# Kernel optimization log

Hardware: AMD Instinct MI355X
Metric: run time of the kernel (lower is better)

Reference implementation:

```python
import jax, jax.numpy as jnp
import numpy as np
from jax import lax

B, S, D, H = 4, 1024, 1024, 16
DK = D // H


def setup_inputs() -> dict:
    key = jax.random.key(0)
    ks = jax.random.split(key, 8)
    s = 0.02
    return {
        "text_embeddings": jax.random.normal(ks[0], (B, S, D), jnp.float32),
        "text_mask": jnp.ones((B, S), jnp.int32),
        "W_G": jax.random.normal(ks[1], (D, D), jnp.float32) * s,
        "b_G": jnp.zeros((D,), jnp.float32),
        "Wq": jax.random.normal(ks[2], (D, D), jnp.float32) * s,
        "bq": jnp.zeros((D,), jnp.float32),
        "Wk": jax.random.normal(ks[3], (D, D), jnp.float32) * s,
        "bk": jnp.zeros((D,), jnp.float32),
        "conv_w": jax.random.normal(ks[4], (D, H, 3), jnp.float32) * s,
        "conv_b": jnp.zeros((D,), jnp.float32),
    }


def _rope_tables(seq_len, dk):
    # interleaved sinusoidal tables, each value repeated twice along feature dim
    pos = jnp.arange(seq_len, dtype=jnp.float32)[:, None]            # [S,1]
    inv = jnp.power(10000.0, -2.0 * jnp.arange(dk // 2, dtype=jnp.float32) / dk)
    ang = pos * inv                                                   # [S,DK/2]
    cos_pos = jnp.repeat(jnp.cos(ang), 2, axis=-1)[None, None]        # [1,1,S,DK]
    sin_pos = jnp.repeat(jnp.sin(ang), 2, axis=-1)[None, None]
    return cos_pos, sin_pos


def reference(text_embeddings, text_mask, W_G, b_G, Wq, bq, Wk, bk, conv_w, conv_b):
    b, s, d = text_embeddings.shape
    g = text_embeddings @ W_G + b_G                                   # [B,S,D]
    q = (g @ Wq + bq).reshape(b, s, H, DK).transpose(0, 2, 1, 3)      # [B,H,S,DK]
    k = (g @ Wk + bk).reshape(b, s, H, DK).transpose(0, 2, 1, 3)

    cos_pos, sin_pos = _rope_tables(s, DK)
    # NOTE: query rotation uses +q_odd (module does NOT negate for q), key uses -k_odd
    qw2 = jnp.stack([q[..., 1::2], q[..., ::2]], axis=-1).reshape(q.shape)
    qw = q * cos_pos + qw2 * sin_pos
    kw2 = jnp.stack([-k[..., 1::2], k[..., ::2]], axis=-1).reshape(k.shape)
    kw = k * cos_pos + kw2 * sin_pos

    scores = jnp.einsum("bhqd,bhkd->bhqk", qw, kw) / np.float32(np.sqrt(DK))
    mask = text_mask[:, None, None, :]                                # [B,1,1,S]
    scores = jnp.where(mask == 0, jnp.float32(-1e9), scores)
    p_attn = jax.nn.softmax(scores, axis=-1)                          # [B,H,S,S]

    row0 = p_attn[:, :, 0, :]                                         # [B,H,S]
    conv = lax.conv_general_dilated(
        row0, conv_w, window_strides=(1,), padding=[(1, 1)],
        dimension_numbers=("NCH", "OIH", "NCH"))                      # [B,D,S]
    return jax.nn.relu(conv + conv_b[None, :, None])
```

## Files before the change

### kernel.cpp

```cpp
#include <hip/hip_runtime.h>
#include <math.h>

#define B_  4
#define S_  1024
#define D_  1024
#define H_  16
#define DK_ 64
#define M_  (B_ * S_)

typedef __bf16 bf16x8 __attribute__((ext_vector_type(8)));
typedef float  f32x4  __attribute__((ext_vector_type(4)));

__device__ __forceinline__ unsigned short f2bf(float f) {
  unsigned u = __builtin_bit_cast(unsigned, f);
  u = (u + 0x7FFFu + ((u >> 16) & 1u)) >> 16;
  return (unsigned short)u;
}
__device__ __forceinline__ float bf2f(unsigned short h) {
  unsigned u = ((unsigned)h) << 16;
  return __builtin_bit_cast(float, u);
}

__device__ __forceinline__ void gl_lds16(const void* g, void* lds) {
  __builtin_amdgcn_global_load_lds(
      (const __attribute__((address_space(1))) unsigned int*)(unsigned long long)g,
      (__attribute__((address_space(3))) unsigned int*)(unsigned int)(unsigned long long)lds,
      16, 0, 0);
}

__global__ __launch_bounds__(256) void prep_kernel(
    const float* __restrict__ X, const float* __restrict__ W_G,
    const float* __restrict__ Wk, const float* __restrict__ bG,
    unsigned short* __restrict__ Xbf, unsigned short* __restrict__ WGbf,
    unsigned short* __restrict__ WkT, float* __restrict__ tab,
    float* __restrict__ partG, float* __restrict__ partB) {
  __shared__ float tle[32][33];
  __shared__ float gs2[4][32];
  __shared__ float bgs[32];
  const int blk = blockIdx.x;
  const int tid = threadIdx.x;

  if (blk < 2048) {
    const int i = (blk * 256 + tid) * 2;
    const float4 v0 = ((const float4*)X)[i];
    const float4 v1 = ((const float4*)X)[i + 1];
    ushort4 h0, h1;
    h0.x = f2bf(v0.x); h0.y = f2bf(v0.y); h0.z = f2bf(v0.z); h0.w = f2bf(v0.w);
    h1.x = f2bf(v1.x); h1.y = f2bf(v1.y); h1.z = f2bf(v1.z); h1.w = f2bf(v1.w);
    ((ushort4*)Xbf)[i] = h0;
    ((ushort4*)Xbf)[i + 1] = h1;
  } else if (blk < 2560) {
    const int i = ((blk - 2048) * 256 + tid) * 2;
    const float4 v0 = ((const float4*)W_G)[i];
    const float4 v1 = ((const float4*)W_G)[i + 1];
    ushort4 h0, h1;
    h0.x = f2bf(v0.x); h0.y = f2bf(v0.y); h0.z = f2bf(v0.z); h0.w = f2bf(v0.w);
    h1.x = f2bf(v1.x); h1.y = f2bf(v1.y); h1.z = f2bf(v1.z); h1.w = f2bf(v1.w);
    ((ushort4*)WGbf)[i] = h0;
    ((ushort4*)WGbf)[i + 1] = h1;
  } else if (blk < 3584) {
    const int t = blk - 2560;
    const int k0 = (t & 31) * 32;
    const int n0 = (t >> 5) * 32;
    const int tx = tid & 31;
    const int ty = tid >> 5;
#pragma unroll
    for (int r = 0; r < 32; r += 8)
      tle[ty + r][tx] = Wk[(size_t)(k0 + ty + r) * 1024 + n0 + tx];
    __syncthreads();
#pragma unroll
    for (int r = 0; r < 32; r += 8)
      WkT[(size_t)(n0 + ty + r) * 1024 + k0 + tx] = f2bf(tle[tx][ty + r]);
  } else if (blk < 3712) {
    const int idx = (blk - 3584) * 256 + tid;
    const int s = idx >> 5, j = idx & 31;
    const float inv = (float)exp(-(double)j * (9.210340371976182736 / 32.0));
    float sn, c;
    sincosf((float)s * inv, &sn, &c);
    tab[(size_t)s * 64 + 2 * j] = c;
    tab[(size_t)s * 64 + 2 * j + 1] = sn;
  } else if (blk < 3840) {
    const int bl = blk - 3712;
    const int sg = bl >> 2;
    const int mg = bl & 3;
    if (tid < 128) {
      const int b = tid >> 5, kk = tid & 31;
      gs2[b][kk] = X[(size_t)b * S_ * D_ + sg * 32 + kk];
    }
    __syncthreads();
    const int mid = mg * 256 + tid;
    float a0 = 0.f, a1 = 0.f, a2 = 0.f, a3 = 0.f;
#pragma unroll
    for (int kk = 0; kk < 32; ++kk) {
      const float w = W_G[(size_t)(sg * 32 + kk) * 1024 + mid];
      a0 = fmaf(gs2[0][kk], w, a0);
      a1 = fmaf(gs2[1][kk], w, a1);
      a2 = fmaf(gs2[2][kk], w, a2);
      a3 = fmaf(gs2[3][kk], w, a3);
    }
    partG[(size_t)(sg * 4 + 0) * 1024 + mid] = a0;
    partG[(size_t)(sg * 4 + 1) * 1024 + mid] = a1;
    partG[(size_t)(sg * 4 + 2) * 1024 + mid] = a2;
    partG[(size_t)(sg * 4 + 3) * 1024 + mid] = a3;
  } else {
    const int bl = blk - 3840;
    const int sl = bl >> 2;
    const int ng = bl & 3;
    if (tid < 32) bgs[tid] = bG[sl * 32 + tid];
    __syncthreads();
    const int n = ng * 256 + tid;
    float a = 0.f;
#pragma unroll
    for (int kk = 0; kk < 32; ++kk)
      a = fmaf(bgs[kk], Wk[(size_t)(sl * 32 + kk) * 1024 + n], a);
    partB[(size_t)sl * 1024 + n] = a;
  }
}

#define GM 64
#define GN 128

__global__ __launch_bounds__(256) void gemm_bf16(
    const unsigned short* __restrict__ A, const unsigned short* __restrict__ BT,
    const float* __restrict__ bias, unsigned short* __restrict__ C,
    const int mShift, const int nGemmBlocks,
    const float* __restrict__ Wq, float* __restrict__ part,
    const float* __restrict__ partG, const float* __restrict__ bG,
    const float* __restrict__ partB, const float* __restrict__ bk,
    float* __restrict__ biasK) {
  __shared__ __align__(16) unsigned short As[2][GM * 32];
  __shared__ __align__(16) unsigned short Bs[2][GN * 32];
  __shared__ float gs[4][32];

  const int flat = blockIdx.x;
  const int tid  = threadIdx.x;

  if (flat >= nGemmBlocks) {
    const int eb = flat - nGemmBlocks;
    if (eb < 128) {
      const int slab = eb >> 2;
      const int n = (eb & 3) * 256 + tid;
      if (tid < 128) {
        const int b = tid >> 5, kk = tid & 31;
        float v = bG[slab * 32 + kk];
        const float* pg = partG + (size_t)b * 1024 + slab * 32 + kk;
#pragma unroll
        for (int sg = 0; sg < 32; ++sg) v += pg[(size_t)sg * 4096];
        gs[b][kk] = v;
      }
      __syncthreads();
      float a0 = 0.f, a1 = 0.f, a2 = 0.f, a3 = 0.f;
#pragma unroll
      for (int kk = 0; kk < 32; ++kk) {
        const float w = Wq[(size_t)(slab * 32 + kk) * D_ + n];
        a0 = fmaf(gs[0][kk], w, a0);
        a1 = fmaf(gs[1][kk], w, a1);
        a2 = fmaf(gs[2][kk], w, a2);
        a3 = fmaf(gs[3][kk], w, a3);
      }
      part[(size_t)(slab * 4 + 0) * D_ + n] = a0;
      part[(size_t)(slab * 4 + 1) * D_ + n] = a1;
      part[(size_t)(slab * 4 + 2) * D_ + n] = a2;
      part[(size_t)(slab * 4 + 3) * D_ + n] = a3;
    } else {
      const int n = (eb - 128) * 256 + tid;
      float v = bk[n];
#pragma unroll
      for (int sl = 0; sl < 32; ++sl) v += partB[(size_t)sl * 1024 + n];
      biasK[n] = v;
    }
    return;
  }

  const int bx = flat >> mShift;
  const int by = flat & ((1 << mShift) - 1);
  const int wv   = tid >> 6;
  const int lane = tid & 63;
  const int m0 = by * GM;
  const int n0 = bx * GN;

  const int colOff = (lane & 3) * 8;
  const size_t aOff  = (size_t)(m0 + 16 * wv + (lane >> 2)) * 1024 + colOff;
  const size_t bOff0 = (size_t)(n0 + 32 * wv + (lane >> 2)) * 1024 + colOff;
  const size_t bOff1 = bOff0 + (size_t)16 * 1024;

  const int l15  = lane & 15;
  const int quad = lane >> 4;

  f32x4 acc[4][2];
#pragma unroll
  for (int i = 0; i < 4; ++i)
#pragma unroll
    for (int j = 0; j < 2; ++j) acc[i][j] = (f32x4){0.f, 0.f, 0.f, 0.f};

#pragma unroll 1
  for (int k0 = 0; k0 < 1024; k0 += 64) {
    __syncthreads();
#pragma unroll
    for (int ks = 0; ks < 2; ++ks) {
      gl_lds16(A  + aOff  + k0 + ks * 32, &As[ks][wv * 512]);
      gl_lds16(BT + bOff0 + k0 + ks * 32, &Bs[ks][wv * 1024]);
      gl_lds16(BT + bOff1 + k0 + ks * 32, &Bs[ks][wv * 1024 + 512]);
    }
    __syncthreads();

#pragma unroll
    for (int ks = 0; ks < 2; ++ks) {
      bf16x8 af[4], bfr[2];
#pragma unroll
      for (int mi = 0; mi < 4; ++mi)
        af[mi] = *(const bf16x8*)(&As[ks][(mi * 16 + l15) * 32 + quad * 8]);
#pragma unroll
      for (int ni = 0; ni < 2; ++ni)
        bfr[ni] =
            *(const bf16x8*)(&Bs[ks][(wv * 32 + ni * 16 + l15) * 32 + quad * 8]);
#pragma unroll
      for (int mi = 0; mi < 4; ++mi)
#pragma unroll
        for (int ni = 0; ni < 2; ++ni)
          acc[mi][ni] = __builtin_amdgcn_mfma_f32_16x16x32_bf16(
              af[mi], bfr[ni], acc[mi][ni], 0, 0, 0);
    }
  }

#pragma unroll
  for (int ni = 0; ni < 2; ++ni) {
    const int n = n0 + wv * 32 + ni * 16 + l15;
    const float bv = bias ? bias[n] : 0.f;
#pragma unroll
    for (int mi = 0; mi < 4; ++mi) {
#pragma unroll
      for (int r = 0; r < 4; ++r) {
        const int m = m0 + mi * 16 + quad * 4 + r;
        C[(size_t)m * 1024 + n] = f2bf(acc[mi][ni][r] + bv);
      }
    }
  }
}

__global__ __launch_bounds__(256) void attn_scores_kernel(
    const unsigned short* __restrict__ Kbf, const float* __restrict__ part,
    const float* __restrict__ bq, const float* __restrict__ tab,
    const int* __restrict__ mask, float* __restrict__ scores,
    float* __restrict__ mS) {
  const int bi = blockIdx.x;
  const int b = bi >> 9;
  const int h = (bi >> 5) & 15;
  const int chunk = bi & 31;
  const int tid = threadIdx.x;
  const int bh = b * H_ + h;
  const int sl = tid >> 3;
  const int j  = tid & 7;
  const int s  = chunk * 32 + sl;

  __shared__ float q0s[DK_];
  __shared__ float wredm[4];
  __shared__ float wreds[4];

  if (tid < 64) {
    const int n = h * DK_ + tid;
    float v = bq[n];
#pragma unroll
    for (int sl2 = 0; sl2 < 32; ++sl2)
      v += part[(size_t)(sl2 * 4 + b) * D_ + n];
    q0s[tid] = v;
  }
  __syncthreads();

  const ushort4* kp =
      (const ushort4*)(Kbf + ((size_t)(b * S_ + s)) * D_ + h * DK_ + j * 8);
  const ushort4 k0 = kp[0], k1 = kp[1];
  const float4* tb = (const float4*)(tab + (size_t)s * 64 + j * 8);
  const float4 t0 = tb[0], t1 = tb[1];

  float dot = 0.f;
  {
    const float ka = bf2f(k0.x), kb = bf2f(k0.y);
    dot += q0s[j * 8 + 0] * (ka * t0.x - kb * t0.y) +
           q0s[j * 8 + 1] * (kb * t0.x + ka * t0.y);
  }
  {
    const float ka = bf2f(k0.z), kb = bf2f(k0.w);
    dot += q0s[j * 8 + 2] * (ka * t0.z - kb * t0.w) +
           q0s[j * 8 + 3] * (kb * t0.z + ka * t0.w);
  }
  {
    const float ka = bf2f(k1.x), kb = bf2f(k1.y);
    dot += q0s[j * 8 + 4] * (ka * t1.x - kb * t1.y) +
           q0s[j * 8 + 5] * (kb * t1.x + ka * t1.y);
  }
  {
    const float ka = bf2f(k1.z), kb = bf2f(k1.w);
    dot += q0s[j * 8 + 6] * (ka * t1.z - kb * t1.w) +
           q0s[j * 8 + 7] * (kb * t1.z + ka * t1.w);
  }
  dot += __shfl_xor(dot, 1);
  dot += __shfl_xor(dot, 2);
  dot += __shfl_xor(dot, 4);
  dot *= 0.125f;
  if (mask[b * S_ + s] == 0) dot = -1e9f;
  if (j == 0) scores[(size_t)bh * S_ + s] = dot;

  float mx = dot;
#pragma unroll
  for (int off = 8; off < 64; off <<= 1) mx = fmaxf(mx, __shfl_xor(mx, off));
  if ((tid & 63) == 0) wredm[tid >> 6] = mx;
  __syncthreads();
  mx = fmaxf(fmaxf(wredm[0], wredm[1]), fmaxf(wredm[2], wredm[3]));

  float e = (j == 0) ? expf(dot - mx) : 0.f;
#pragma unroll
  for (int off = 1; off < 64; off <<= 1) e += __shfl_xor(e, off);
  if ((tid & 63) == 0) wreds[tid >> 6] = e;
  __syncthreads();
  if (tid == 0) {
    mS[(size_t)(bh * 32 + chunk) * 2 + 0] = mx;
    mS[(size_t)(bh * 32 + chunk) * 2 + 1] =
        wreds[0] + wreds[1] + wreds[2] + wreds[3];
  }
}

__global__ __launch_bounds__(256) void conv_norm_relu_kernel(
    const float* __restrict__ scores, const float* __restrict__ mS,
    const float* __restrict__ cw, const float* __restrict__ cb,
    float* __restrict__ out) {
  const int b  = blockIdx.y;
  const int s0 = blockIdx.x * 128;
  const int o0 = blockIdx.z * 128;
  const int tid = threadIdx.x;
  const int tx = tid & 15;
  const int ty = tid >> 4;

  __shared__ float msh[16], ish[16];
  __shared__ __align__(16) float wT[48][128];
  __shared__ float cbs[128];
  __shared__ __align__(16) float pm[16][132];

  if (tid < 16) {
    const int bh = b * H_ + tid;
    float m = -3e38f;
#pragma unroll
    for (int c = 0; c < 32; ++c)
      m = fmaxf(m, mS[(size_t)(bh * 32 + c) * 2]);
    float S = 0.f;
#pragma unroll
    for (int c = 0; c < 32; ++c)
      S += mS[(size_t)(bh * 32 + c) * 2 + 1] *
           expf(mS[(size_t)(bh * 32 + c) * 2] - m);
    msh[tid] = m;
    ish[tid] = 1.f / S;
  }
  for (int i = tid; i < 128 * 48; i += 256) {
    const int ol = i / 48, ct = i % 48;
    wT[ct][ol] = cw[(size_t)(o0 + ol) * 48 + ct];
  }
  if (tid < 128) cbs[tid] = cb[o0 + tid];
  __syncthreads();

  for (int i = tid; i < 16 * 130; i += 256) {
    const int c = i / 130, ss = i % 130;
    const int gs = s0 - 1 + ss;
    pm[c][ss] = (gs >= 0 && gs < S_)
                    ? expf(scores[(size_t)(b * H_ + c) * S_ + gs] - msh[c]) *
                          ish[c]
                    : 0.f;
  }
  __syncthreads();

  float acc[8][8];
#pragma unroll
  for (int i = 0; i < 8; ++i) {
    const float cv = cbs[ty * 8 + i];
#pragma unroll
    for (int j = 0; j < 8; ++j) acc[i][j] = cv;
  }

#pragma unroll
  for (int c = 0; c < 16; ++c) {
    float p[12];
    *(float4*)(p + 0) = *(const float4*)&pm[c][tx * 8 + 0];
    *(float4*)(p + 4) = *(const float4*)&pm[c][tx * 8 + 4];
    *(float4*)(p + 8) = *(const float4*)&pm[c][tx * 8 + 8];
#pragma unroll
    for (int t = 0; t < 3; ++t) {
      float w[8];
      *(float4*)(w + 0) = *(const float4*)&wT[c * 3 + t][ty * 8 + 0];
      *(float4*)(w + 4) = *(const float4*)&wT[c * 3 + t][ty * 8 + 4];
#pragma unroll
      for (int i = 0; i < 8; ++i)
#pragma unroll
        for (int j = 0; j < 8; ++j)
          acc[i][j] = fmaf(p[j + t], w[i], acc[i][j]);
    }
  }

#pragma unroll
  for (int i = 0; i < 8; ++i) {
    float* orow =
        out + ((size_t)b * D_ + o0 + ty * 8 + i) * S_ + s0 + tx * 8;
    float4 v0, v1;
    v0.x = fmaxf(acc[i][0], 0.f); v0.y = fmaxf(acc[i][1], 0.f);
    v0.z = fmaxf(acc[i][2], 0.f); v0.w = fmaxf(acc[i][3], 0.f);
    v1.x = fmaxf(acc[i][4], 0.f); v1.y = fmaxf(acc[i][5], 0.f);
    v1.z = fmaxf(acc[i][6], 0.f); v1.w = fmaxf(acc[i][7], 0.f);
    *(float4*)(orow + 0) = v0;
    *(float4*)(orow + 4) = v1;
  }
}

extern "C" void kernel_launch(void* const* d_in, const int* in_sizes, int n_in,
                              void* d_out, int out_size, void* d_ws,
                              size_t ws_size, hipStream_t stream) {
  const float* x    = (const float*)d_in[0];
  const int*   mask = (const int*)d_in[1];
  const float* W_G  = (const float*)d_in[2];
  const float* b_G  = (const float*)d_in[3];
  const float* Wq   = (const float*)d_in[4];
  const float* bq   = (const float*)d_in[5];
  const float* Wk   = (const float*)d_in[6];
  const float* bk   = (const float*)d_in[7];
  const float* cw   = (const float*)d_in[8];
  const float* cb   = (const float*)d_in[9];
  float* out = (float*)d_out;

  char* ws = (char*)d_ws;
  unsigned short* Xbf  = (unsigned short*)(ws);
  unsigned short* Kbf  = (unsigned short*)(ws + (8u << 20));
  unsigned short* WkT  = (unsigned short*)(ws + (16u << 20));
  unsigned short* WGbf = (unsigned short*)(ws + (18u << 20));
  unsigned short* WfT  = (unsigned short*)(ws + (20u << 20));
  float* part   = (float*)(ws + (22u << 20));
  float* partG  = (float*)(ws + (22u << 20) + (512u << 10));
  float* partB  = (float*)(ws + (23u << 20));
  float* biasK  = (float*)(ws + (23u << 20) + (128u << 10));
  float* ropeT  = (float*)(ws + (23u << 20) + (256u << 10));
  float* scores = (float*)(ws + (23u << 20) + (512u << 10));
  float* mS     = (float*)(ws + (23u << 20) + (768u << 10));

  prep_kernel<<<3968, 256, 0, stream>>>(x, W_G, Wk, b_G, Xbf, WGbf, WkT,
                                        ropeT, partG, partB);
  gemm_bf16<<<260, 256, 0, stream>>>(WkT, WGbf, nullptr, WfT, 4, 128,
                                     Wq, part, partG, b_G, partB, bk, biasK);
  gemm_bf16<<<512, 256, 0, stream>>>(Xbf, WfT, biasK, Kbf, 6, 512,
                                     nullptr, nullptr, nullptr, nullptr,
                                     nullptr, nullptr, nullptr);
  attn_scores_kernel<<<2048, 256, 0, stream>>>(Kbf, part, bq, ropeT, mask,
                                               scores, mS);
  conv_norm_relu_kernel<<<dim3(8, B_, 8), 256, 0, stream>>>(
      scores, mS, cw, cb, out);
}
```

Baseline: 149.9 us.

## Fuse RoPE query-row scoring and softmax stats into K-projection GEMM epilogue

```diff
diff --git a/kernel.cpp b/kernel.cpp
--- a/kernel.cpp
+++ b/kernel.cpp
@@ -31,8 +31,7 @@
 __global__ __launch_bounds__(256) void prep_kernel(
     const float* __restrict__ X, const float* __restrict__ W_G,
     const float* __restrict__ Wk, const float* __restrict__ bG,
-    unsigned short* __restrict__ Xbf, unsigned short* __restrict__ WGbf,
-    unsigned short* __restrict__ WkT, float* __restrict__ tab,
+    unsigned short* __restrict__ WGbf, unsigned short* __restrict__ WkT,
     float* __restrict__ partG, float* __restrict__ partB) {
   __shared__ float tle[32][33];
   __shared__ float gs2[4][32];
@@ -40,17 +39,8 @@
   const int blk = blockIdx.x;
   const int tid = threadIdx.x;
 
-  if (blk < 2048) {
+  if (blk < 512) {
     const int i = (blk * 256 + tid) * 2;
-    const float4 v0 = ((const float4*)X)[i];
-    const float4 v1 = ((const float4*)X)[i + 1];
-    ushort4 h0, h1;
-    h0.x = f2bf(v0.x); h0.y = f2bf(v0.y); h0.z = f2bf(v0.z); h0.w = f2bf(v0.w);
-    h1.x = f2bf(v1.x); h1.y = f2bf(v1.y); h1.z = f2bf(v1.z); h1.w = f2bf(v1.w);
-    ((ushort4*)Xbf)[i] = h0;
-    ((ushort4*)Xbf)[i + 1] = h1;
-  } else if (blk < 2560) {
-    const int i = ((blk - 2048) * 256 + tid) * 2;
     const float4 v0 = ((const float4*)W_G)[i];
     const float4 v1 = ((const float4*)W_G)[i + 1];
     ushort4 h0, h1;
@@ -58,8 +48,8 @@
     h1.x = f2bf(v1.x); h1.y = f2bf(v1.y); h1.z = f2bf(v1.z); h1.w = f2bf(v1.w);
     ((ushort4*)WGbf)[i] = h0;
     ((ushort4*)WGbf)[i + 1] = h1;
-  } else if (blk < 3584) {
-    const int t = blk - 2560;
+  } else if (blk < 1536) {
+    const int t = blk - 512;
     const int k0 = (t & 31) * 32;
     const int n0 = (t >> 5) * 32;
     const int tx = tid & 31;
@@ -71,16 +61,8 @@
 #pragma unroll
     for (int r = 0; r < 32; r += 8)
       WkT[(size_t)(n0 + ty + r) * 1024 + k0 + tx] = f2bf(tle[tx][ty + r]);
-  } else if (blk < 3712) {
-    const int idx = (blk - 3584) * 256 + tid;
-    const int s = idx >> 5, j = idx & 31;
-    const float inv = (float)exp(-(double)j * (9.210340371976182736 / 32.0));
-    float sn, c;
-    sincosf((float)s * inv, &sn, &c);
-    tab[(size_t)s * 64 + 2 * j] = c;
-    tab[(size_t)s * 64 + 2 * j + 1] = sn;
-  } else if (blk < 3840) {
-    const int bl = blk - 3712;
+  } else if (blk < 1664) {
+    const int bl = blk - 1536;
     const int sg = bl >> 2;
     const int mg = bl & 3;
     if (tid < 128) {
@@ -103,7 +85,7 @@
     partG[(size_t)(sg * 4 + 2) * 1024 + mid] = a2;
     partG[(size_t)(sg * 4 + 3) * 1024 + mid] = a3;
   } else {
-    const int bl = blk - 3840;
+    const int bl = blk - 1664;
     const int sl = bl >> 2;
     const int ng = bl & 3;
     if (tid < 32) bgs[tid] = bG[sl * 32 + tid];
@@ -127,10 +109,16 @@
     const float* __restrict__ Wq, float* __restrict__ part,
     const float* __restrict__ partG, const float* __restrict__ bG,
     const float* __restrict__ partB, const float* __restrict__ bk,
-    float* __restrict__ biasK) {
+    float* __restrict__ biasK,
+    const float* __restrict__ X, unsigned short* __restrict__ Xbf,
+    float* __restrict__ tab,
+    const float* __restrict__ bq, const int* __restrict__ mask,
+    float* __restrict__ scores, float* __restrict__ mS) {
   __shared__ __align__(16) unsigned short As[2][GM * 32];
   __shared__ __align__(16) unsigned short Bs[2][GN * 32];
   __shared__ float gs[4][32];
+  __shared__ float q0s[128];
+  __shared__ float sc[64][9];
 
   const int flat = blockIdx.x;
   const int tid  = threadIdx.x;
@@ -162,12 +150,29 @@
       part[(size_t)(slab * 4 + 1) * D_ + n] = a1;
       part[(size_t)(slab * 4 + 2) * D_ + n] = a2;
       part[(size_t)(slab * 4 + 3) * D_ + n] = a3;
-    } else {
+    } else if (eb < 132) {
       const int n = (eb - 128) * 256 + tid;
       float v = bk[n];
 #pragma unroll
       for (int sl = 0; sl < 32; ++sl) v += partB[(size_t)sl * 1024 + n];
       biasK[n] = v;
+    } else if (eb < 260) {
+      const int idx = (eb - 132) * 256 + tid;
+      const int s = idx >> 5, j = idx & 31;
+      const float inv = (float)exp(-(double)j * (9.210340371976182736 / 32.0));
+      float sn, c;
+      sincosf((float)s * inv, &sn, &c);
+      tab[(size_t)s * 64 + 2 * j] = c;
+      tab[(size_t)s * 64 + 2 * j + 1] = sn;
+    } else {
+      const int i = ((eb - 260) * 256 + tid) * 2;
+      const float4 v0 = ((const float4*)X)[i];
+      const float4 v1 = ((const float4*)X)[i + 1];
+      ushort4 h0, h1;
+      h0.x = f2bf(v0.x); h0.y = f2bf(v0.y); h0.z = f2bf(v0.z); h0.w = f2bf(v0.w);
+      h1.x = f2bf(v1.x); h1.y = f2bf(v1.y); h1.z = f2bf(v1.z); h1.w = f2bf(v1.w);
+      ((ushort4*)Xbf)[i] = h0;
+      ((ushort4*)Xbf)[i + 1] = h1;
     }
     return;
   }
@@ -179,6 +184,15 @@
   const int m0 = by * GM;
   const int n0 = bx * GN;
 
+  if (scores && tid < 128) {
+    const int nq = n0 + tid;
+    float v = bq[nq];
+#pragma unroll
+    for (int sl2 = 0; sl2 < 32; ++sl2)
+      v += part[(size_t)(sl2 * 4 + (m0 >> 10)) * D_ + nq];
+    q0s[tid] = v;
+  }
+
   const int colOff = (lane & 3) * 8;
   const size_t aOff  = (size_t)(m0 + 16 * wv + (lane >> 2)) * 1024 + colOff;
   const size_t bOff0 = (size_t)(n0 + 32 * wv + (lane >> 2)) * 1024 + colOff;
@@ -223,6 +237,62 @@
     }
   }
 
+  if (scores) {
+    const int b_i   = m0 >> 10;
+    const int sbase = m0 & 1023;
+#pragma unroll
+    for (int ni = 0; ni < 2; ++ni) {
+      const int n_loc = wv * 32 + ni * 16 + l15;
+      const float bv  = bias[n0 + n_loc];
+      const float q0a = q0s[n_loc];
+      const float q0b = q0s[n_loc ^ 1];
+      const float sq  = (n_loc & 1) ? -q0b : q0b;
+      const int j2    = (n_loc & 63) & ~1;
+#pragma unroll
+      for (int mi = 0; mi < 4; ++mi) {
+#pragma unroll
+        for (int r = 0; r < 4; ++r) {
+          const int s_loc = mi * 16 + quad * 4 + r;
+          const float2 cs =
+              *(const float2*)(tab + (size_t)(sbase + s_loc) * 64 + j2);
+          const float coef = q0a * cs.x + sq * cs.y;
+          float v = (acc[mi][ni][r] + bv) * coef;
+          v += __shfl_xor(v, 1);
+          v += __shfl_xor(v, 2);
+          v += __shfl_xor(v, 4);
+          v += __shfl_xor(v, 8);
+          if (l15 == 0) sc[s_loc][wv * 2 + ni] = v;
+        }
+      }
+    }
+    __syncthreads();
+    if (tid < 128) {
+      const int h_loc = tid >> 6;
+      const int s_loc = tid & 63;
+      const float* row = sc[s_loc];
+      float dot = (row[h_loc * 4 + 0] + row[h_loc * 4 + 1]) +
+                  (row[h_loc * 4 + 2] + row[h_loc * 4 + 3]);
+      dot *= 0.125f;
+      const int s = sbase + s_loc;
+      if (mask[b_i * S_ + s] == 0) dot = -1e9f;
+      const int bh = b_i * H_ + (bx * 2 + h_loc);
+      scores[(size_t)bh * S_ + s] = dot;
+      float mx = dot;
+#pragma unroll
+      for (int off = 16; off >= 1; off >>= 1)
+        mx = fmaxf(mx, __shfl_xor(mx, off, 32));
+      float e = expf(dot - mx);
+#pragma unroll
+      for (int off = 16; off >= 1; off >>= 1) e += __shfl_xor(e, off, 32);
+      if ((s_loc & 31) == 0) {
+        const int ch = ((by & 15) << 1) + (s_loc >> 5);
+        mS[((size_t)bh * 32 + ch) * 2 + 0] = mx;
+        mS[((size_t)bh * 32 + ch) * 2 + 1] = e;
+      }
+    }
+    return;
+  }
+
 #pragma unroll
   for (int ni = 0; ni < 2; ++ni) {
     const int n = n0 + wv * 32 + ni * 16 + l15;
@@ -235,88 +305,6 @@
         C[(size_t)m * 1024 + n] = f2bf(acc[mi][ni][r] + bv);
       }
     }
-  }
-}
-
-__global__ __launch_bounds__(256) void attn_scores_kernel(
-    const unsigned short* __restrict__ Kbf, const float* __restrict__ part,
-    const float* __restrict__ bq, const float* __restrict__ tab,
-    const int* __restrict__ mask, float* __restrict__ scores,
-    float* __restrict__ mS) {
-  const int bi = blockIdx.x;
-  const int b = bi >> 9;
-  const int h = (bi >> 5) & 15;
-  const int chunk = bi & 31;
-  const int tid = threadIdx.x;
-  const int bh = b * H_ + h;
-  const int sl = tid >> 3;
-  const int j  = tid & 7;
-  const int s  = chunk * 32 + sl;
-
-  __shared__ float q0s[DK_];
-  __shared__ float wredm[4];
-  __shared__ float wreds[4];
-
-  if (tid < 64) {
-    const int n = h * DK_ + tid;
-    float v = bq[n];
-#pragma unroll
-    for (int sl2 = 0; sl2 < 32; ++sl2)
-      v += part[(size_t)(sl2 * 4 + b) * D_ + n];
-    q0s[tid] = v;
-  }
-  __syncthreads();
-
-  const ushort4* kp =
-      (const ushort4*)(Kbf + ((size_t)(b * S_ + s)) * D_ + h * DK_ + j * 8);
-  const ushort4 k0 = kp[0], k1 = kp[1];
-  const float4* tb = (const float4*)(tab + (size_t)s * 64 + j * 8);
-  const float4 t0 = tb[0], t1 = tb[1];
-
-  float dot = 0.f;
-  {
-    const float ka = bf2f(k0.x), kb = bf2f(k0.y);
-    dot += q0s[j * 8 + 0] * (ka * t0.x - kb * t0.y) +
-           q0s[j * 8 + 1] * (kb * t0.x + ka * t0.y);
-  }
-  {
-    const float ka = bf2f(k0.z), kb = bf2f(k0.w);
-    dot += q0s[j * 8 + 2] * (ka * t0.z - kb * t0.w) +
-           q0s[j * 8 + 3] * (kb * t0.z + ka * t0.w);
-  }
-  {
-    const float ka = bf2f(k1.x), kb = bf2f(k1.y);
-    dot += q0s[j * 8 + 4] * (ka * t1.x - kb * t1.y) +
-           q0s[j * 8 + 5] * (kb * t1.x + ka * t1.y);
-  }
-  {
-    const float ka = bf2f(k1.z), kb = bf2f(k1.w);
-    dot += q0s[j * 8 + 6] * (ka * t1.z - kb * t1.w) +
-           q0s[j * 8 + 7] * (kb * t1.z + ka * t1.w);
-  }
-  dot += __shfl_xor(dot, 1);
-  dot += __shfl_xor(dot, 2);
-  dot += __shfl_xor(dot, 4);
-  dot *= 0.125f;
-  if (mask[b * S_ + s] == 0) dot = -1e9f;
-  if (j == 0) scores[(size_t)bh * S_ + s] = dot;
-
-  float mx = dot;
-#pragma unroll
-  for (int off = 8; off < 64; off <<= 1) mx = fmaxf(mx, __shfl_xor(mx, off));
-  if ((tid & 63) == 0) wredm[tid >> 6] = mx;
-  __syncthreads();
-  mx = fmaxf(fmaxf(wredm[0], wredm[1]), fmaxf(wredm[2], wredm[3]));
-
-  float e = (j == 0) ? expf(dot - mx) : 0.f;
-#pragma unroll
-  for (int off = 1; off < 64; off <<= 1) e += __shfl_xor(e, off);
-  if ((tid & 63) == 0) wreds[tid >> 6] = e;
-  __syncthreads();
-  if (tid == 0) {
-    mS[(size_t)(bh * 32 + chunk) * 2 + 0] = mx;
-    mS[(size_t)(bh * 32 + chunk) * 2 + 1] =
-        wreds[0] + wreds[1] + wreds[2] + wreds[3];
   }
 }
 
@@ -425,7 +413,6 @@
 
   char* ws = (char*)d_ws;
   unsigned short* Xbf  = (unsigned short*)(ws);
-  unsigned short* Kbf  = (unsigned short*)(ws + (8u << 20));
   unsigned short* WkT  = (unsigned short*)(ws + (16u << 20));
   unsigned short* WGbf = (unsigned short*)(ws + (18u << 20));
   unsigned short* WfT  = (unsigned short*)(ws + (20u << 20));
@@ -437,15 +424,17 @@
   float* scores = (float*)(ws + (23u << 20) + (512u << 10));
   float* mS     = (float*)(ws + (23u << 20) + (768u << 10));
 
-  prep_kernel<<<3968, 256, 0, stream>>>(x, W_G, Wk, b_G, Xbf, WGbf, WkT,
-                                        ropeT, partG, partB);
-  gemm_bf16<<<260, 256, 0, stream>>>(WkT, WGbf, nullptr, WfT, 4, 128,
-                                     Wq, part, partG, b_G, partB, bk, biasK);
-  gemm_bf16<<<512, 256, 0, stream>>>(Xbf, WfT, biasK, Kbf, 6, 512,
-                                     nullptr, nullptr, nullptr, nullptr,
-                                     nullptr, nullptr, nullptr);
-  attn_scores_kernel<<<2048, 256, 0, stream>>>(Kbf, part, bq, ropeT, mask,
-                                               scores, mS);
+  prep_kernel<<<1792, 256, 0, stream>>>(x, W_G, Wk, b_G, WGbf, WkT,
+                                        partG, partB);
+  gemm_bf16<<<2436, 256, 0, stream>>>(WkT, WGbf, nullptr, WfT, 4, 128,
+                                      Wq, part, partG, b_G, partB, bk, biasK,
+                                      x, Xbf, ropeT,
+                                      nullptr, nullptr, nullptr, nullptr);
+  gemm_bf16<<<512, 256, 0, stream>>>(Xbf, WfT, biasK, nullptr, 6, 512,
+                                     nullptr, part, nullptr, nullptr,
+                                     nullptr, nullptr, nullptr,
+                                     nullptr, nullptr, ropeT,
+                                     bq, mask, scores, mS);
   conv_norm_relu_kernel<<<dim3(8, B_, 8), 256, 0, stream>>>(
       scores, mS, cw, cb, out);
 }
```

Result: slower. 153.0 us (+2.0%).
